# Kernel optimization log

Hardware: AMD Instinct MI355X
Metric: run time of the kernel (lower is better)

The kernel has to match this reference:

```python
import jax, jax.numpy as jnp
import numpy as np

N_HEADS = 16


def setup_inputs() -> dict:
    key = jax.random.key(0)
    k1, k2, k3, k4, k5 = jax.random.split(key, 5)
    B, S, D = 2, 2048, 1024
    return {
        "query": jax.random.normal(k1, (B, S, D), dtype=jnp.float32),
        "key": jax.random.normal(k2, (B, S, D), dtype=jnp.float32),
        "value": jax.random.normal(k3, (B, S, D), dtype=jnp.float32),
        "fc_w": jax.random.normal(k4, (D, D), dtype=jnp.float32) * (1.0 / np.sqrt(D)),
        "fc_b": jax.random.normal(k5, (D,), dtype=jnp.float32) * 0.01,
    }


def reference(query, key, value, fc_w, fc_b):
    b, s, d = query.shape
    head_dim = d // N_HEADS
    q = query.reshape(b, s, N_HEADS, head_dim)
    k = key.reshape(b, s, N_HEADS, head_dim)
    v = value.reshape(b, s, N_HEADS, head_dim)
    # energy: [b, n, q, k]
    energy = jnp.einsum('bqnd,bknd->bnqk', q, k)
    scale = 1.0 / jnp.sqrt(jnp.asarray(head_dim, dtype=energy.dtype))
    attn = jax.nn.softmax(energy * scale, axis=3)
    out = jnp.einsum('bnqk,bknd->bqnd', attn, v).reshape(b, s, d)
    # fc: y = x @ W^T + b (torch Linear convention)
    return out @ fc_w.T + fc_b
```

## Files before the change

### kernel.cpp

```cpp
#include <hip/hip_runtime.h>
#include <hip/hip_bf16.h>

#define BATCH 2
#define SEQ 2048
#define DMODEL 1024
#define NHEADS 16
#define HDIM 64
#define KVBLK 64
#define NCHUNK (SEQ / KVBLK)
#define NITER (NCHUNK / 2)

#define QSCALE 0.180336880f
#define DEFER_THR 8.0f

typedef __bf16 bf16x8 __attribute__((ext_vector_type(8)));
typedef __bf16 bf16x4 __attribute__((ext_vector_type(4)));
typedef float f32x4 __attribute__((ext_vector_type(4)));
typedef float f32x16 __attribute__((ext_vector_type(16)));
typedef unsigned int uint2v __attribute__((ext_vector_type(2)));

union B8u { unsigned int u[4]; bf16x8 v; };

__device__ __forceinline__ unsigned int cvt_pk_bf16(float lo, float hi) {
  unsigned int d;
  asm("v_cvt_pk_bf16_f32 %0, %1, %2" : "=v"(d) : "v"(lo), "v"(hi));
  return d;
}

__device__ __forceinline__ void permlane32_swap(unsigned &a, unsigned &b) {
  auto r = __builtin_amdgcn_permlane32_swap(a, b, false, false);
  unsigned tmp[2];
  __builtin_memcpy(tmp, &r, 8);
  a = tmp[0]; b = tmp[1];
}

__global__ __launch_bounds__(256)
void conv_all(const float* __restrict__ K, __bf16* __restrict__ Kbf,
              const float* __restrict__ V, __bf16* __restrict__ Vt,
              const float* __restrict__ W, __bf16* __restrict__ Wbf) {
  const int p = blockIdx.x;
  __shared__ __bf16 T[64][72];

  if (p < 2048) {
    const int t = p * 256 + threadIdx.x;
    const int d8 = t & 7, key = (t >> 3) & (SEQ - 1), g = t >> 14;
    const float* src = K + ((size_t)(g >> 4) * SEQ + key) * DMODEL +
                       (g & 15) * HDIM + d8 * 8;
    f32x4 a = *reinterpret_cast<const f32x4*>(src);
    f32x4 c = *reinterpret_cast<const f32x4*>(src + 4);
    bf16x8 o;
#pragma unroll
    for (int j = 0; j < 4; ++j) { o[j] = (__bf16)a[j]; o[4 + j] = (__bf16)c[j]; }
    *reinterpret_cast<bf16x8*>(Kbf + (size_t)t * 8) = o;
  } else if (p < 3072) {
    const int blk = p - 2048;
    const int g = blk >> 5, c0 = (blk & 31) * 64;
    const int b = g >> 4, h = g & 15;
    {
      const int key = threadIdx.x >> 2, dq = threadIdx.x & 3;
      const float* src = V + ((size_t)(b * SEQ) + c0 + key) * DMODEL +
                         h * HDIM + dq * 16;
#pragma unroll
      for (int i = 0; i < 4; ++i) {
        f32x4 v = *reinterpret_cast<const f32x4*>(src + 4 * i);
        bf16x4 o;
#pragma unroll
        for (int j = 0; j < 4; ++j) o[j] = (__bf16)v[j];
        *reinterpret_cast<bf16x4*>(&T[key][dq * 16 + 4 * i]) = o;
      }
    }
    __syncthreads();
    {
      const int d = threadIdx.x >> 2, kq = threadIdx.x & 3;
      bf16x8 r0, r1;
#pragma unroll
      for (int i = 0; i < 8; ++i) {
        r0[i] = T[kq * 16 + i][d];
        r1[i] = T[kq * 16 + 8 + i][d];
      }
      __bf16* dst = Vt + ((size_t)g * HDIM + d) * SEQ + c0 + kq * 16;
      *reinterpret_cast<bf16x8*>(dst) = r0;
      *reinterpret_cast<bf16x8*>(dst + 8) = r1;
    }
  } else {
    const int t = (p - 3072) * 256 + threadIdx.x;
    f32x4 a = *reinterpret_cast<const f32x4*>(W + (size_t)t * 8);
    f32x4 c = *reinterpret_cast<const f32x4*>(W + (size_t)t * 8 + 4);
    bf16x8 o;
#pragma unroll
    for (int j = 0; j < 4; ++j) { o[j] = (__bf16)a[j]; o[4 + j] = (__bf16)c[j]; }
    *reinterpret_cast<bf16x8*>(Wbf + (size_t)t * 8) = o;
  }
}

__global__ __launch_bounds__(512, 4)
void attn_kernel(const float* __restrict__ Q, const __bf16* __restrict__ Kbf,
                 const __bf16* __restrict__ Vt, __bf16* __restrict__ O) {
  const int p = blockIdx.x;
  const int xcd = p & 7, slot = p >> 3;
  const int g = xcd + 8 * (slot >> 4);
  const int b = g >> 4, h = g & 15;
  const int q0 = (slot & 15) * 128;

  const int tid = threadIdx.x;
  const int wave = tid >> 6, lane = tid & 63;
  const int qg = wave & 3, ks = wave >> 2;
  const int l31 = lane & 31, hi = lane >> 5;
  const int ob = hi << 4;
  const int swz = (l31 & 7) << 4;

  __shared__ __align__(16) __bf16 KsA[2][2][64 * 64];
  __shared__ __align__(16) __bf16 VtA[2][2][64 * 64];

  const int qrow = q0 + (qg << 5) + l31;
  const float* qp = Q + ((size_t)(b * SEQ + qrow)) * DMODEL + h * HDIM;
  bf16x8 qf[4];
#pragma unroll
  for (int kd = 0; kd < 4; ++kd) {
    f32x4 a = *reinterpret_cast<const f32x4*>(qp + kd * 16 + hi * 8);
    f32x4 c = *reinterpret_cast<const f32x4*>(qp + kd * 16 + hi * 8 + 4);
#pragma unroll
    for (int j = 0; j < 4; ++j) {
      qf[kd][j]     = (__bf16)(a[j] * QSCALE);
      qf[kd][4 + j] = (__bf16)(c[j] * QSCALE);
    }
  }

  f32x16 oacc0, oacc1;
#pragma unroll
  for (int r = 0; r < 16; ++r) { oacc0[r] = 0.f; oacc1[r] = 0.f; }
  float m_run = -1e30f, l_run = 0.f;

  const __bf16* kgb = Kbf + (size_t)g * SEQ * HDIM;
  const __bf16* vgb = Vt + (size_t)g * HDIM * SEQ;

  const int t2 = tid & 255;
  const int sk_key = t2 >> 2, sk_dq = t2 & 3;
  const int sv_dim = t2 >> 2, sv_kq = t2 & 3;
  const int ksw = (sk_key & 7) << 4;
  const int vsw = (sv_dim & 7) << 4;

  bf16x8 kr0, kr1, vr0, vr1;

#define STAGE_LOAD(C0)                                                        \
  do {                                                                        \
    const __bf16* kc = kgb + (size_t)(C0 + sk_key) * HDIM + sk_dq * 16;       \
    kr0 = *reinterpret_cast<const bf16x8*>(kc);                               \
    kr1 = *reinterpret_cast<const bf16x8*>(kc + 8);                           \
    const __bf16* vc = vgb + (size_t)sv_dim * SEQ + (C0) + sv_kq * 16;        \
    vr0 = *reinterpret_cast<const bf16x8*>(vc);                               \
    vr1 = *reinterpret_cast<const bf16x8*>(vc + 8);                           \
  } while (0)

#define STAGE_WRITE(B)                                                        \
  do {                                                                        \
    char* kdst = (char*)(&KsA[ks][B][0]) + sk_key * 128;                      \
    *reinterpret_cast<bf16x8*>(kdst + (((sk_dq << 5)) ^ ksw)) = kr0;          \
    *reinterpret_cast<bf16x8*>(kdst + (((sk_dq << 5) | 16) ^ ksw)) = kr1;     \
    char* vdst = (char*)(&VtA[ks][B][0]) + sv_dim * 128;                      \
    *reinterpret_cast<bf16x8*>(vdst + (((sv_kq << 5)) ^ vsw)) = vr0;          \
    *reinterpret_cast<bf16x8*>(vdst + (((sv_kq << 5) | 16) ^ vsw)) = vr1;     \
  } while (0)

  STAGE_LOAD(ks * NITER * KVBLK);
  STAGE_WRITE(0);
  __syncthreads();

  for (int i = 0; i < NITER; ++i) {
    const int cur = i & 1;
    const bool pf = (i + 1 < NITER);
    if (pf) STAGE_LOAD((ks * NITER + i + 1) * KVBLK);

    const char* kb = (const char*)(&KsA[ks][cur][0]);
    const char* vb = (const char*)(&VtA[ks][cur][0]);

    f32x16 s0, s1;
#pragma unroll
    for (int r = 0; r < 16; ++r) { s0[r] = 0.f; s1[r] = 0.f; }
    __builtin_amdgcn_s_setprio(1);
#pragma unroll
    for (int kd = 0; kd < 4; ++kd) {
      bf16x8 a0 = *reinterpret_cast<const bf16x8*>(
          kb + l31 * 128 + (((kd << 5) | ob) ^ swz));
      bf16x8 a1 = *reinterpret_cast<const bf16x8*>(
          kb + (32 + l31) * 128 + (((kd << 5) | ob) ^ swz));
      s0 = __builtin_amdgcn_mfma_f32_32x32x16_bf16(a0, qf[kd], s0, 0, 0, 0);
      s1 = __builtin_amdgcn_mfma_f32_32x32x16_bf16(a1, qf[kd], s1, 0, 0, 0);
    }
    __builtin_amdgcn_s_setprio(0);

    float m8[8];
#pragma unroll
    for (int r = 0; r < 8; ++r)
      m8[r] = fmaxf(fmaxf(s0[r], s0[r + 8]), fmaxf(s1[r], s1[r + 8]));
    float pm = fmaxf(fmaxf(fmaxf(m8[0], m8[1]), fmaxf(m8[2], m8[3])),
                     fmaxf(fmaxf(m8[4], m8[5]), fmaxf(m8[6], m8[7])));
    pm = fmaxf(pm, __shfl_xor(pm, 32, 64));

    if (!__all(pm <= m_run + DEFER_THR)) {
      float mu = fmaxf(m_run, pm);
      float al = __builtin_amdgcn_exp2f(m_run - mu);
      m_run = mu;
      l_run *= al;
#pragma unroll
      for (int r = 0; r < 16; ++r) { oacc0[r] *= al; oacc1[r] *= al; }
    }

#pragma unroll
    for (int r = 0; r < 16; ++r) {
      s0[r] = __builtin_amdgcn_exp2f(s0[r] - m_run);
      s1[r] = __builtin_amdgcn_exp2f(s1[r] - m_run);
    }
    float t8[8];
#pragma unroll
    for (int r = 0; r < 8; ++r)
      t8[r] = (s0[r] + s0[r + 8]) + (s1[r] + s1[r + 8]);
    float ts = ((t8[0] + t8[1]) + (t8[2] + t8[3])) +
               ((t8[4] + t8[5]) + (t8[6] + t8[7]));
    ts += __shfl_xor(ts, 32, 64);
    l_run += ts;

    B8u pfr[4];
#pragma unroll
    for (int kq = 0; kq < 4; ++kq) {
      f32x16 ps = (kq < 2) ? s0 : s1;
      const int r0 = (kq & 1) * 8;
      unsigned lo0 = cvt_pk_bf16(ps[r0 + 0], ps[r0 + 1]);
      unsigned lo1 = cvt_pk_bf16(ps[r0 + 2], ps[r0 + 3]);
      unsigned h0  = cvt_pk_bf16(ps[r0 + 4], ps[r0 + 5]);
      unsigned h1  = cvt_pk_bf16(ps[r0 + 6], ps[r0 + 7]);
      permlane32_swap(lo0, h0);
      permlane32_swap(lo1, h1);
      pfr[kq].u[0] = lo0; pfr[kq].u[1] = lo1;
      pfr[kq].u[2] = h0;  pfr[kq].u[3] = h1;
    }

    __builtin_amdgcn_s_setprio(1);
#pragma unroll
    for (int kq = 0; kq < 4; ++kq) {
      bf16x8 v0 = *reinterpret_cast<const bf16x8*>(
          vb + l31 * 128 + (((kq << 5) | ob) ^ swz));
      bf16x8 v1 = *reinterpret_cast<const bf16x8*>(
          vb + (32 + l31) * 128 + (((kq << 5) | ob) ^ swz));
      oacc0 = __builtin_amdgcn_mfma_f32_32x32x16_bf16(v0, pfr[kq].v, oacc0, 0, 0, 0);
      oacc1 = __builtin_amdgcn_mfma_f32_32x32x16_bf16(v1, pfr[kq].v, oacc1, 0, 0, 0);
    }
    __builtin_amdgcn_s_setprio(0);

    if (pf) STAGE_WRITE(cur ^ 1);
    __syncthreads();
  }

  float* Ob = (float*)&KsA[0][0][0];
  float* mb = (float*)&VtA[0][0][0];
  float* lb = mb + 4 * 32;

  if (ks == 1) {
    if (hi == 0) { mb[qg * 32 + l31] = m_run; lb[qg * 32 + l31] = l_run; }
#pragma unroll
    for (int dt = 0; dt < 2; ++dt) {
      f32x16 oa = dt ? oacc1 : oacc0;
#pragma unroll
      for (int r = 0; r < 16; ++r) {
        int dim = dt * 32 + (r & 3) + 8 * (r >> 2) + 4 * hi;
        Ob[(qg * 64 + dim) * 32 + l31] = oa[r];
      }
    }
  }
  __syncthreads();

  if (ks == 0) {
    float m1 = mb[qg * 32 + l31], l1 = lb[qg * 32 + l31];
    float m = fmaxf(m_run, m1);
    float a0 = __builtin_amdgcn_exp2f(m_run - m);
    float a1 = __builtin_amdgcn_exp2f(m1 - m);
    const float inv = 1.0f / (a0 * l_run + a1 * l1);
    __bf16* op = O + ((size_t)(b * SEQ + qrow)) * DMODEL + h * HDIM;
#pragma unroll
    for (int dt = 0; dt < 2; ++dt) {
      f32x16 oa = dt ? oacc1 : oacc0;
#pragma unroll
      for (int a = 0; a < 4; ++a) {
        float e[4];
#pragma unroll
        for (int j = 0; j < 4; ++j) {
          int r = 4 * a + j;
          int dim = dt * 32 + (r & 3) + 8 * (r >> 2) + 4 * hi;
          float opart = Ob[(qg * 64 + dim) * 32 + l31];
          e[j] = (oa[r] * a0 + opart * a1) * inv;
        }
        uint2v w;
        w[0] = cvt_pk_bf16(e[0], e[1]);
        w[1] = cvt_pk_bf16(e[2], e[3]);
        *reinterpret_cast<uint2v*>((char*)op + (dt * 32 + a * 8 + hi * 4) * 2) = w;
      }
    }
  }
#undef STAGE_LOAD
#undef STAGE_WRITE
}

__global__ __launch_bounds__(256)
void fc_kernel(const __bf16* __restrict__ X, const __bf16* __restrict__ W,
               const float* __restrict__ bias, float* __restrict__ Y) {
  const int p = blockIdx.x;
  const int xcd = p & 7, slot = p >> 3;
  const int m0 = (xcd + 8 * (slot >> 4)) * 128;
  const int n0 = (slot & 15) * 64;

  const int tid = threadIdx.x;
  const int wave = tid >> 6, lane = tid & 63;
  const int g = lane >> 4, lr = lane & 15;
  const int wm = wave >> 1, wn = wave & 1;

  __shared__ __bf16 As[128][72];
  __shared__ __bf16 Bs[64][72];

  f32x4 acc[4][2];
#pragma unroll
  for (int i = 0; i < 4; ++i)
#pragma unroll
    for (int j = 0; j < 2; ++j) acc[i][j] = (f32x4){0.f, 0.f, 0.f, 0.f};

  float bv[2];
#pragma unroll
  for (int j = 0; j < 2; ++j) bv[j] = bias[n0 + wn * 32 + 16 * j + lr];

  for (int kk = 0; kk < DMODEL; kk += 64) {
    __syncthreads();
#pragma unroll
    for (int e = 0; e < 4; ++e) {
      int idx = tid + 256 * e;
      int row = idx >> 3, k8 = idx & 7;
      bf16x8 v = *reinterpret_cast<const bf16x8*>(
          X + (size_t)(m0 + row) * DMODEL + kk + k8 * 8);
      *reinterpret_cast<bf16x8*>(&As[row][k8 * 8]) = v;
    }
#pragma unroll
    for (int e = 0; e < 2; ++e) {
      int idx = tid + 256 * e;
      int row = idx >> 3, k8 = idx & 7;
      bf16x8 w = *reinterpret_cast<const bf16x8*>(
          W + (size_t)(n0 + row) * DMODEL + kk + k8 * 8);
      *reinterpret_cast<bf16x8*>(&Bs[row][k8 * 8]) = w;
    }
    __syncthreads();

#pragma unroll
    for (int ks2 = 0; ks2 < 2; ++ks2) {
      bf16x8 af[4], bfr[2];
#pragma unroll
      for (int i = 0; i < 4; ++i)
        af[i] = *reinterpret_cast<const bf16x8*>(
            &As[wm * 64 + 16 * i + lr][ks2 * 32 + g * 8]);
#pragma unroll
      for (int j = 0; j < 2; ++j)
        bfr[j] = *reinterpret_cast<const bf16x8*>(
            &Bs[wn * 32 + 16 * j + lr][ks2 * 32 + g * 8]);
#pragma unroll
      for (int i = 0; i < 4; ++i)
#pragma unroll
        for (int j = 0; j < 2; ++j)
          acc[i][j] = __builtin_amdgcn_mfma_f32_16x16x32_bf16(
              af[i], bfr[j], acc[i][j], 0, 0, 0);
    }
  }

#pragma unroll
  for (int i = 0; i < 4; ++i) {
    int m = m0 + wm * 64 + 16 * i + g * 4;
#pragma unroll
    for (int j = 0; j < 2; ++j) {
      int n = n0 + wn * 32 + 16 * j + lr;
      float* yp = Y + (size_t)m * DMODEL + n;
#pragma unroll
      for (int r = 0; r < 4; ++r) yp[(size_t)r * DMODEL] = acc[i][j][r] + bv[j];
    }
  }
}

extern "C" void kernel_launch(void* const* d_in, const int* in_sizes, int n_in,
                              void* d_out, int out_size, void* d_ws, size_t ws_size,
                              hipStream_t stream) {
  const float* q    = (const float*)d_in[0];
  const float* k    = (const float*)d_in[1];
  const float* v    = (const float*)d_in[2];
  const float* w    = (const float*)d_in[3];
  const float* bias = (const float*)d_in[4];
  float* out = (float*)d_out;

  char* ws = (char*)d_ws;
  __bf16* O   = (__bf16*)(ws);
  __bf16* Kbf = (__bf16*)(ws + (8u << 20));
  __bf16* Vt  = (__bf16*)(ws + (16u << 20));
  __bf16* Wbf = (__bf16*)(ws + (24u << 20));

  conv_all<<<dim3(3584), 256, 0, stream>>>(k, Kbf, v, Vt, w, Wbf);
  attn_kernel<<<dim3(512), 512, 0, stream>>>(q, Kbf, Vt, O);
  fc_kernel<<<dim3(512), 256, 0, stream>>>(O, Wbf, bias, out);
}
```

Before: 85.14 us.

## Load K/V MFMA fragments directly from global memory, drop LDS staging

Removes the double-buffered LDS staging of K and V tiles and the per-iteration __syncthreads, and has each wave read its MFMA operand fragments straight from global memory (relying on L2/L1 reuse across the four query-group waves). This is meant to cut LDS traffic, barriers and shared-memory footprint, which may raise occupancy. The cost is roughly four times more global/L1 load requests, since each wave fetches the same K/V chunk, and the loads are no longer prefetched an iteration ahead, so latency can be exposed.

New measurement: 168.0 us. +97.3%, slower.

```diff
diff --git a/kernel.cpp b/kernel.cpp
--- a/kernel.cpp
+++ b/kernel.cpp
@@ -106,11 +106,9 @@
   const int wave = tid >> 6, lane = tid & 63;
   const int qg = wave & 3, ks = wave >> 2;
   const int l31 = lane & 31, hi = lane >> 5;
-  const int ob = hi << 4;
-  const int swz = (l31 & 7) << 4;
-
-  __shared__ __align__(16) __bf16 KsA[2][2][64 * 64];
-  __shared__ __align__(16) __bf16 VtA[2][2][64 * 64];
+
+  __shared__ float Ob[4][64][32];
+  __shared__ float mlb[2][4][32];
 
   const int qrow = q0 + (qg << 5) + l31;
   const float* qp = Q + ((size_t)(b * SEQ + qrow)) * DMODEL + h * HDIM;
@@ -131,48 +129,20 @@
   for (int r = 0; r < 16; ++r) { oacc0[r] = 0.f; oacc1[r] = 0.f; }
   float m_run = -1e30f, l_run = 0.f;
 
-  const __bf16* kgb = Kbf + (size_t)g * SEQ * HDIM;
-  const __bf16* vgb = Vt + (size_t)g * HDIM * SEQ;
-
-  const int t2 = tid & 255;
-  const int sk_key = t2 >> 2, sk_dq = t2 & 3;
-  const int sv_dim = t2 >> 2, sv_kq = t2 & 3;
-  const int ksw = (sk_key & 7) << 4;
-  const int vsw = (sv_dim & 7) << 4;
-
-  bf16x8 kr0, kr1, vr0, vr1;
-
-#define STAGE_LOAD(C0)                                                        \
-  do {                                                                        \
-    const __bf16* kc = kgb + (size_t)(C0 + sk_key) * HDIM + sk_dq * 16;       \
-    kr0 = *reinterpret_cast<const bf16x8*>(kc);                               \
-    kr1 = *reinterpret_cast<const bf16x8*>(kc + 8);                           \
-    const __bf16* vc = vgb + (size_t)sv_dim * SEQ + (C0) + sv_kq * 16;        \
-    vr0 = *reinterpret_cast<const bf16x8*>(vc);                               \
-    vr1 = *reinterpret_cast<const bf16x8*>(vc + 8);                           \
-  } while (0)
-
-#define STAGE_WRITE(B)                                                        \
-  do {                                                                        \
-    char* kdst = (char*)(&KsA[ks][B][0]) + sk_key * 128;                      \
-    *reinterpret_cast<bf16x8*>(kdst + (((sk_dq << 5)) ^ ksw)) = kr0;          \
-    *reinterpret_cast<bf16x8*>(kdst + (((sk_dq << 5) | 16) ^ ksw)) = kr1;     \
-    char* vdst = (char*)(&VtA[ks][B][0]) + sv_dim * 128;                      \
-    *reinterpret_cast<bf16x8*>(vdst + (((sv_kq << 5)) ^ vsw)) = vr0;          \
-    *reinterpret_cast<bf16x8*>(vdst + (((sv_kq << 5) | 16) ^ vsw)) = vr1;     \
-  } while (0)
-
-  STAGE_LOAD(ks * NITER * KVBLK);
-  STAGE_WRITE(0);
-  __syncthreads();
+  const __bf16* kp0 = Kbf + (size_t)g * SEQ * HDIM + (size_t)l31 * HDIM + hi * 8;
+  const __bf16* kp1 = kp0 + (size_t)32 * HDIM;
+  const __bf16* vp0 = Vt + (size_t)g * HDIM * SEQ + (size_t)l31 * SEQ + hi * 8;
+  const __bf16* vp1 = vp0 + (size_t)32 * SEQ;
 
   for (int i = 0; i < NITER; ++i) {
-    const int cur = i & 1;
-    const bool pf = (i + 1 < NITER);
-    if (pf) STAGE_LOAD((ks * NITER + i + 1) * KVBLK);
-
-    const char* kb = (const char*)(&KsA[ks][cur][0]);
-    const char* vb = (const char*)(&VtA[ks][cur][0]);
+    const int c0 = (ks * NITER + i) * KVBLK;
+
+    bf16x8 ka0[4], ka1[4];
+#pragma unroll
+    for (int kd = 0; kd < 4; ++kd) {
+      ka0[kd] = *reinterpret_cast<const bf16x8*>(kp0 + (size_t)c0 * HDIM + kd * 16);
+      ka1[kd] = *reinterpret_cast<const bf16x8*>(kp1 + (size_t)c0 * HDIM + kd * 16);
+    }
 
     f32x16 s0, s1;
 #pragma unroll
@@ -180,14 +150,17 @@
     __builtin_amdgcn_s_setprio(1);
 #pragma unroll
     for (int kd = 0; kd < 4; ++kd) {
-      bf16x8 a0 = *reinterpret_cast<const bf16x8*>(
-          kb + l31 * 128 + (((kd << 5) | ob) ^ swz));
-      bf16x8 a1 = *reinterpret_cast<const bf16x8*>(
-          kb + (32 + l31) * 128 + (((kd << 5) | ob) ^ swz));
-      s0 = __builtin_amdgcn_mfma_f32_32x32x16_bf16(a0, qf[kd], s0, 0, 0, 0);
-      s1 = __builtin_amdgcn_mfma_f32_32x32x16_bf16(a1, qf[kd], s1, 0, 0, 0);
+      s0 = __builtin_amdgcn_mfma_f32_32x32x16_bf16(ka0[kd], qf[kd], s0, 0, 0, 0);
+      s1 = __builtin_amdgcn_mfma_f32_32x32x16_bf16(ka1[kd], qf[kd], s1, 0, 0, 0);
     }
     __builtin_amdgcn_s_setprio(0);
+
+    bf16x8 va0[4], va1[4];
+#pragma unroll
+    for (int kq = 0; kq < 4; ++kq) {
+      va0[kq] = *reinterpret_cast<const bf16x8*>(vp0 + c0 + kq * 16);
+      va1[kq] = *reinterpret_cast<const bf16x8*>(vp1 + c0 + kq * 16);
+    }
 
     float m8[8];
 #pragma unroll
@@ -238,39 +211,28 @@
     __builtin_amdgcn_s_setprio(1);
 #pragma unroll
     for (int kq = 0; kq < 4; ++kq) {
-      bf16x8 v0 = *reinterpret_cast<const bf16x8*>(
-          vb + l31 * 128 + (((kq << 5) | ob) ^ swz));
-      bf16x8 v1 = *reinterpret_cast<const bf16x8*>(
-          vb + (32 + l31) * 128 + (((kq << 5) | ob) ^ swz));
-      oacc0 = __builtin_amdgcn_mfma_f32_32x32x16_bf16(v0, pfr[kq].v, oacc0, 0, 0, 0);
-      oacc1 = __builtin_amdgcn_mfma_f32_32x32x16_bf16(v1, pfr[kq].v, oacc1, 0, 0, 0);
+      oacc0 = __builtin_amdgcn_mfma_f32_32x32x16_bf16(va0[kq], pfr[kq].v, oacc0, 0, 0, 0);
+      oacc1 = __builtin_amdgcn_mfma_f32_32x32x16_bf16(va1[kq], pfr[kq].v, oacc1, 0, 0, 0);
     }
     __builtin_amdgcn_s_setprio(0);
-
-    if (pf) STAGE_WRITE(cur ^ 1);
-    __syncthreads();
-  }
-
-  float* Ob = (float*)&KsA[0][0][0];
-  float* mb = (float*)&VtA[0][0][0];
-  float* lb = mb + 4 * 32;
+  }
 
   if (ks == 1) {
-    if (hi == 0) { mb[qg * 32 + l31] = m_run; lb[qg * 32 + l31] = l_run; }
+    if (hi == 0) { mlb[0][qg][l31] = m_run; mlb[1][qg][l31] = l_run; }
 #pragma unroll
     for (int dt = 0; dt < 2; ++dt) {
       f32x16 oa = dt ? oacc1 : oacc0;
 #pragma unroll
       for (int r = 0; r < 16; ++r) {
         int dim = dt * 32 + (r & 3) + 8 * (r >> 2) + 4 * hi;
-        Ob[(qg * 64 + dim) * 32 + l31] = oa[r];
+        Ob[qg][dim][l31] = oa[r];
       }
     }
   }
   __syncthreads();
 
   if (ks == 0) {
-    float m1 = mb[qg * 32 + l31], l1 = lb[qg * 32 + l31];
+    float m1 = mlb[0][qg][l31], l1 = mlb[1][qg][l31];
     float m = fmaxf(m_run, m1);
     float a0 = __builtin_amdgcn_exp2f(m_run - m);
     float a1 = __builtin_amdgcn_exp2f(m1 - m);
@@ -286,7 +248,7 @@
         for (int j = 0; j < 4; ++j) {
           int r = 4 * a + j;
           int dim = dt * 32 + (r & 3) + 8 * (r >> 2) + 4 * hi;
-          float opart = Ob[(qg * 64 + dim) * 32 + l31];
+          float opart = Ob[qg][dim][l31];
           e[j] = (oa[r] * a0 + opart * a1) * inv;
         }
         uint2v w;
@@ -296,8 +258,6 @@
       }
     }
   }
-#undef STAGE_LOAD
-#undef STAGE_WRITE
 }
 
 __global__ __launch_bounds__(256)
```
